# Kernel tuning notes

Measured on AMD Instinct MI355X. Metric: run time of the kernel, lower is better.

## Reference

```python
import jax, jax.numpy as jnp
import numpy as np

B, N, CIN, CV, D, H, HD, W, SHIFT = 1024, 192, 63, 27, 256, 8, 32, 8, 4
DEPTH, MLP = 2, 256  # mlp_dim = int(embed_dim * mlp_ratio) = 256


def setup_inputs() -> dict:
    key = jax.random.key(0)
    ks = iter(jax.random.split(key, 64))
    def w(*shape):
        return jax.random.normal(next(ks), shape, jnp.float32) * 0.02
    z = lambda *s: jnp.zeros(s, jnp.float32)
    o = lambda *s: jnp.ones(s, jnp.float32)
    return {
        'input_pts': jax.random.normal(next(ks), (B, N, CIN), jnp.float32),
        'input_views': jax.random.normal(next(ks), (B, CV), jnp.float32),
        'w_in': w(CIN, D), 'b_in': z(D),
        'ln_in_s': o(D), 'ln_in_b': z(D),
        'ln1_s': o(DEPTH, D), 'ln1_b': z(DEPTH, D),
        'wq': w(DEPTH, D, H, HD), 'bq': z(DEPTH, H, HD),
        'wk': w(DEPTH, D, H, HD), 'bk': z(DEPTH, H, HD),
        'wv': w(DEPTH, D, H, HD), 'bv': z(DEPTH, H, HD),
        'wo': w(DEPTH, H, HD, D), 'bo': z(DEPTH, D),
        'ln2_s': o(DEPTH, D), 'ln2_b': z(DEPTH, D),
        'w_mlp1': w(DEPTH, D, MLP), 'b_mlp1': z(DEPTH, MLP),
        'w_mlp2': w(DEPTH, MLP, D), 'b_mlp2': z(DEPTH, D),
        'w_skip': w(DEPTH, CIN + D, D), 'b_skip': z(DEPTH, D),
        'ln_f_s': o(D), 'ln_f_b': z(D),
        'w_alpha': w(D, 1), 'b_alpha': z(1),
        'w_feat': w(D, D), 'b_feat': z(D),
        'w_rgb1': w(D + CV, D // 2), 'b_rgb1': z(D // 2),
        'w_rgb2': w(D // 2, 3), 'b_rgb2': z(3),
    }


def _ln(x, s, b, eps=1e-6):
    m = jnp.mean(x, -1, keepdims=True)
    v = jnp.mean(jnp.square(x - m), -1, keepdims=True)
    return (x - m) * jax.lax.rsqrt(v + eps) * s + b


def _pos_embed(n, d):
    pos = jnp.arange(n, dtype=jnp.float32)[:, None]
    i = jnp.arange(d)
    ang = pos / jnp.power(10000.0, (2 * (i // 2)).astype(jnp.float32) / d)
    return jnp.where(i % 2 == 0, jnp.sin(ang), jnp.cos(ang))[None]  # [1, n, d]


def _block(x, shifted, ln1_s, ln1_b, wq, bq, wk, bk, wv, bv, wo, bo,
           ln2_s, ln2_b, w1, b1, w2, b2):
    b, n, c = x.shape
    y = _ln(x, ln1_s, ln1_b)
    if shifted:
        y = jnp.roll(y, -SHIFT, axis=1)
    yw = y.reshape(b * (n // W), W, c)  # window partition
    q = jnp.einsum('bnc,chd->bnhd', yw, wq) + bq
    k = jnp.einsum('bnc,chd->bnhd', yw, wk) + bk
    v = jnp.einsum('bnc,chd->bnhd', yw, wv) + bv
    scale = np.float32(1.0 / np.sqrt(HD))
    a = jax.nn.softmax(jnp.einsum('bqhd,bkhd->bhqk', q * scale, k), axis=-1)
    o = jnp.einsum('bhqk,bkhd->bqhd', a, v)
    o = jnp.einsum('bqhd,hdc->bqc', o, wo) + bo
    o = o.reshape(b, n, c)  # window reverse
    if shifted:
        o = jnp.roll(o, SHIFT, axis=1)
    x = x + o
    y = _ln(x, ln2_s, ln2_b)
    y = jax.nn.gelu(jnp.einsum('bnc,cm->bnm', y, w1) + b1)
    y = jnp.einsum('bnm,mc->bnc', y, w2) + b2
    return x + y


def reference(input_pts, input_views, w_in, b_in, ln_in_s, ln_in_b,
              ln1_s, ln1_b, wq, bq, wk, bk, wv, bv, wo, bo, ln2_s, ln2_b,
              w_mlp1, b_mlp1, w_mlp2, b_mlp2, w_skip, b_skip,
              ln_f_s, ln_f_b, w_alpha, b_alpha, w_feat, b_feat,
              w_rgb1, b_rgb1, w_rgb2, b_rgb2):
    x = input_pts @ w_in + b_in
    x = _ln(x, ln_in_s, ln_in_b)
    x = x + _pos_embed(x.shape[1], x.shape[2])
    for i in range(DEPTH):  # shift on odd layers; skips = [0, 1]
        x = _block(x, i % 2 == 1, ln1_s[i], ln1_b[i], wq[i], bq[i], wk[i], bk[i],
                   wv[i], bv[i], wo[i], bo[i], ln2_s[i], ln2_b[i],
                   w_mlp1[i], b_mlp1[i], w_mlp2[i], b_mlp2[i])
        x = jax.nn.gelu(jnp.concatenate([input_pts, x], -1) @ w_skip[i] + b_skip[i])
    h = _ln(x, ln_f_s, ln_f_b)
    alpha = h @ w_alpha + b_alpha
    feature = h @ w_feat + b_feat
    views = jnp.repeat(input_views[:, None, :], h.shape[1], axis=1)
    hr = jnp.concatenate([feature, views], -1)
    rgb = jax.nn.gelu(hr @ w_rgb1 + b_rgb1) @ w_rgb2 + b_rgb2
    return rgb, alpha
```

## Files before the change

kernel.cpp:

```cpp
#include <hip/hip_runtime.h>
#include <hip/hip_bf16.h>
#include <math.h>

typedef __hip_bfloat16 bf16;
typedef __attribute__((ext_vector_type(8))) short short8;
typedef __attribute__((ext_vector_type(4))) float f32x4;

#define T_TOK 196608
#define NSEQ  192
#define DMODEL 256
#define CHUNKS 4
#define CHUNKM (T_TOK/CHUNKS)

__device__ __forceinline__ float cvt(float v){ return v; }
__device__ __forceinline__ float cvt(bf16 v){ return __bfloat162float(v); }
__device__ __forceinline__ short bfbits(float f){
  bf16 h = __float2bfloat16(f); return *reinterpret_cast<short*>(&h);
}
__device__ __forceinline__ float blo(unsigned u){ return __uint_as_float(u << 16); }
__device__ __forceinline__ float bhi(unsigned u){ return __uint_as_float(u & 0xffff0000u); }
__device__ __forceinline__ float bfu(unsigned short v){ return __uint_as_float(((unsigned)v) << 16); }
__device__ __forceinline__ unsigned pack2(float a, float b){
  return ((unsigned)(unsigned short)bfbits(a)) | (((unsigned)(unsigned short)bfbits(b)) << 16);
}

__device__ __forceinline__ float gelu_f(float x){
  const float k0 = 0.7978845608028654f;
  return 0.5f*x*(1.0f + tanhf(k0*(x + 0.044715f*x*x*x)));
}

__global__ __launch_bounds__(256) void pe_kernel(float* __restrict__ PE){
  int n = blockIdx.x, d = threadIdx.x;
  float e = (float)(2*(d>>1)) / 256.f;
  float ang = (float)n * powf(10000.f, -e);
  PE[n*DMODEL + d] = (d & 1) ? cosf(ang) : sinf(ang);
}

__global__ __launch_bounds__(256) void w2b_kernel(
    const float* __restrict__ src, bf16* __restrict__ dst,
    int K, int N, int KL, int dstStride, int kOff)
{
  int idx = blockIdx.x*256 + threadIdx.x;
  if (idx >= N*KL) return;
  int n = idx / KL, k = idx - n*KL;
  dst[(size_t)n*dstStride + kOff + k] =
      __float2bfloat16(k < K ? src[(size_t)k*N + n] : 0.f);
}

__global__ __launch_bounds__(256) void pts2b_kernel(
    const float* __restrict__ src, bf16* __restrict__ dst)
{
  int idx = blockIdx.x*256 + threadIdx.x;
  int t = idx >> 6, k = idx & 63;
  dst[idx] = __float2bfloat16(k < 63 ? src[(size_t)t*63 + k] : 0.f);
}

__global__ __launch_bounds__(256) void views2b_kernel(
    const float* __restrict__ src, bf16* __restrict__ dst)
{
  int idx = blockIdx.x*256 + threadIdx.x;
  int t = idx >> 5, k = idx & 31;
  dst[idx] = __float2bfloat16(k < 27 ? src[(size_t)t*27 + k] : 0.f);
}

__global__ __launch_bounds__(256) void biascat_kernel(
    const float* __restrict__ b0, const float* __restrict__ b1,
    const float* __restrict__ b2, float* __restrict__ dst)
{
  int tid = threadIdx.x;
  const float* s = (blockIdx.x == 0) ? b0 : (blockIdx.x == 1) ? b1 : b2;
  dst[blockIdx.x*256 + tid] = s[tid];
}

__global__ __launch_bounds__(256) void ln_pe_kernel(
    bf16* __restrict__ X, const float* __restrict__ s, const float* __restrict__ b,
    const float* __restrict__ PE, float* __restrict__ s1o, float* __restrict__ s2o)
{
  const int lane = threadIdx.x & 63, w = threadIdx.x >> 6;
  const size_t t = (size_t)blockIdx.x * 4 + w;
  const int n = (int)(t % NSEQ);
  const int c = lane * 4;

  ushort4 u = *reinterpret_cast<const ushort4*>(X + t*DMODEL + c);
  float x0 = bfu(u.x), x1 = bfu(u.y), x2 = bfu(u.z), x3 = bfu(u.w);

  float sx = x0 + x1 + x2 + x3;
  float sq = x0*x0 + x1*x1 + x2*x2 + x3*x3;
  #pragma unroll
  for (int off = 32; off; off >>= 1){
    sx += __shfl_xor(sx, off, 64);
    sq += __shfl_xor(sq, off, 64);
  }
  float mean = sx * (1.f/256.f);
  float var  = sq * (1.f/256.f) - mean*mean;
  float rstd = rsqrtf(var + 1e-6f);

  float4 sv = *reinterpret_cast<const float4*>(s + c);
  float4 bv = *reinterpret_cast<const float4*>(b + c);
  float4 pv = *reinterpret_cast<const float4*>(PE + n*DMODEL + c);

  float y0 = (x0 - mean)*rstd*sv.x + bv.x + pv.x;
  float y1 = (x1 - mean)*rstd*sv.y + bv.y + pv.y;
  float y2 = (x2 - mean)*rstd*sv.z + bv.z + pv.z;
  float y3 = (x3 - mean)*rstd*sv.w + bv.w + pv.w;

  ushort4 o;
  o.x = (unsigned short)bfbits(y0);
  o.y = (unsigned short)bfbits(y1);
  o.z = (unsigned short)bfbits(y2);
  o.w = (unsigned short)bfbits(y3);
  *reinterpret_cast<ushort4*>(X + t*DMODEL + c) = o;

  float sy  = y0 + y1 + y2 + y3;
  float syq = y0*y0 + y1*y1 + y2*y2 + y3*y3;
  #pragma unroll
  for (int off = 32; off; off >>= 1){
    sy  += __shfl_xor(sy,  off, 64);
    syq += __shfl_xor(syq, off, 64);
  }
  if (lane == 0){ s1o[t] = sy; s2o[t] = syq; }
}

template<int MODE, bool ADD, bool GELU, bool STATS>
__global__ __launch_bounds__(256) void gemm_mfma(
    const bf16* __restrict__ A1, int lda1,
    const bf16* __restrict__ A2, int lda2, int SB, int aOff,
    const float* __restrict__ s1i, const float* __restrict__ s2i,
    const float* __restrict__ lnS, const float* __restrict__ lnB,
    const bf16* __restrict__ WT, int Kpad, const float* __restrict__ bias,
    bf16* __restrict__ C, int ldc, size_t segStride, int cOff, int rollShift,
    float* __restrict__ s1o, float* __restrict__ s2o)
{
  __shared__ short As[128*40];
  __shared__ short Cs[128*136];
  const int tid = threadIdx.x;
  const int lane = tid & 63, wid = tid >> 6;
  const int wm = wid >> 1, wn = wid & 1;
  const int col16 = lane & 15, quad = lane >> 4;
  const int m0 = blockIdx.y * 128, n0 = blockIdx.x * 128;
  const int sm = tid >> 1, half = tid & 1;

  f32x4 acc[4][4];
  #pragma unroll
  for (int i = 0; i < 4; i++)
    #pragma unroll
    for (int j = 0; j < 4; j++) acc[i][j] = (f32x4){0.f,0.f,0.f,0.f};

  int row = m0 + sm;
  if (MODE <= 1 && rollShift){
    int bb = row / NSEQ;
    int n  = row - bb*NSEQ;
    n += rollShift; if (n >= NSEQ) n -= NSEQ;
    row = bb*NSEQ + n;
  }
  const size_t arow = (size_t)aOff + row;
  const size_t arow2 = (MODE == 3) ? (arow / NSEQ) : arow;
  float lnMu = 0.f, lnRs = 0.f;
  if (MODE == 1){
    float m1 = s1i[arow] * (1.f/256.f);
    float m2 = s2i[arow] * (1.f/256.f);
    lnMu = m1;
    lnRs = rsqrtf(m2 - m1*m1 + 1e-6f);
  }

  for (int k0 = 0; k0 < Kpad; k0 += 32){
    const int gk = k0 + half*16;
    if (MODE == 1){
      const uint4 u0 = *(const uint4*)(A1 + arow*lda1 + gk);
      const uint4 u1 = *(const uint4*)(A1 + arow*lda1 + gk + 8);
      const unsigned uu[8] = {u0.x,u0.y,u0.z,u0.w,u1.x,u1.y,u1.z,u1.w};
      unsigned out[8];
      #pragma unroll
      for (int p = 0; p < 8; p++){
        int g = gk + 2*p;
        float a = (blo(uu[p]) - lnMu) * lnRs * lnS[g]   + lnB[g];
        float b = (bhi(uu[p]) - lnMu) * lnRs * lnS[g+1] + lnB[g+1];
        out[p] = pack2(a, b);
      }
      *(uint4*)&As[sm*40 + half*16]     = *(uint4*)&out[0];
      *(uint4*)&As[sm*40 + half*16 + 8] = *(uint4*)&out[4];
    } else {
      const bf16* src;
      if (MODE == 0) src = A1 + arow*lda1 + gk;
      else src = (gk < SB) ? (A1 + arow*(size_t)lda1 + gk)
                           : (A2 + arow2*(size_t)lda2 + (gk - SB));
      const uint4 u0 = *(const uint4*)(src);
      const uint4 u1 = *(const uint4*)(src + 8);
      *(uint4*)&As[sm*40 + half*16]     = u0;
      *(uint4*)&As[sm*40 + half*16 + 8] = u1;
    }
    __syncthreads();

    short8 afr[4];
    #pragma unroll
    for (int mi = 0; mi < 4; mi++)
      afr[mi] = *(const short8*)&As[(wm*64 + mi*16 + col16)*40 + quad*8];
    short8 bfr[4];
    #pragma unroll
    for (int ni = 0; ni < 4; ni++)
      bfr[ni] = *(const short8*)((const short*)WT
                 + (size_t)(n0 + wn*64 + ni*16 + col16)*Kpad + k0 + quad*8);
    #pragma unroll
    for (int mi = 0; mi < 4; mi++)
      #pragma unroll
      for (int ni = 0; ni < 4; ni++)
        acc[mi][ni] = __builtin_amdgcn_mfma_f32_16x16x32_bf16(
            afr[mi], bfr[ni], acc[mi][ni], 0, 0, 0);
    __syncthreads();
  }

  #pragma unroll
  for (int ni = 0; ni < 4; ni++){
    int ncol = wn*64 + ni*16 + col16;
    float bv = bias[n0 + ncol];
    #pragma unroll
    for (int mi = 0; mi < 4; mi++){
      f32x4 a = acc[mi][ni];
      #pragma unroll
      for (int r = 0; r < 4; r++){
        int lrow = wm*64 + mi*16 + quad*4 + r;
        float val = a[r] + bv;
        if (GELU) val = gelu_f(val);
        Cs[lrow*136 + ncol] = bfbits(val);
      }
    }
  }
  __syncthreads();

  const int seg = n0 >> 8;
  const int nb  = n0 & 255;
  const int orow = tid >> 4;
  const int ocol = (tid & 15) * 8;
  #pragma unroll
  for (int p = 0; p < 8; p++){
    int lrow = p*16 + orow;
    size_t mrow = (size_t)cOff + m0 + lrow;
    short8 v = *(const short8*)&Cs[lrow*136 + ocol];
    bf16* dst = C + (size_t)seg*segStride + mrow*ldc + nb + ocol;
    float rowSum = 0.f, rowSq = 0.f;
    if (ADD){
      short8 c = *(const short8*)dst;
      short8 o;
      #pragma unroll
      for (int e = 0; e < 8; e++){
        bf16 va, ca;
        *reinterpret_cast<short*>(&va) = v[e];
        *reinterpret_cast<short*>(&ca) = c[e];
        float f = cvt(va) + cvt(ca);
        o[e] = bfbits(f);
        if (STATS){ rowSum += f; rowSq += f*f; }
      }
      *(short8*)dst = o;
    } else {
      if (STATS){
        #pragma unroll
        for (int e = 0; e < 8; e++){
          bf16 va; *reinterpret_cast<short*>(&va) = v[e];
          float f = cvt(va);
          rowSum += f; rowSq += f*f;
        }
      }
      *(short8*)dst = v;
    }
    if (STATS){
      #pragma unroll
      for (int mk = 1; mk <= 8; mk <<= 1){
        rowSum += __shfl_xor(rowSum, mk, 64);
        rowSq  += __shfl_xor(rowSq,  mk, 64);
      }
      if ((tid & 15) == 0){
        atomicAdd(&s1o[mrow], rowSum);
        atomicAdd(&s2o[mrow], rowSq);
      }
    }
  }
}

__global__ __launch_bounds__(256) void attn_lite(
    bf16* __restrict__ Qg, const bf16* __restrict__ Kg, const bf16* __restrict__ Vg)
{
  __shared__ float qs[8][257], ks[8][257], vs[8][257];
  __shared__ float sc[8][8][8];
  const int c = threadIdx.x;
  const size_t base = (size_t)blockIdx.x * 8 * 256;
  #pragma unroll
  for (int j = 0; j < 8; j++){
    qs[j][c] = cvt(Qg[base + j*256 + c]);
    ks[j][c] = cvt(Kg[base + j*256 + c]);
    vs[j][c] = cvt(Vg[base + j*256 + c]);
  }
  __syncthreads();

  const float scale = 0.17677669529663687f;
  #pragma unroll
  for (int r = 0; r < 2; r++){
    int idx = r*256 + c;
    int h = idx >> 6, qi = (idx >> 3) & 7, ki = idx & 7;
    float s = 0.f;
    #pragma unroll
    for (int d = 0; d < 32; d++) s += qs[qi][h*32+d] * ks[ki][h*32+d];
    sc[h][qi][ki] = s * scale;
  }
  __syncthreads();

  if (c < 64){
    int h = c >> 3, qi = c & 7;
    float mx = -1e30f;
    #pragma unroll
    for (int u = 0; u < 8; u++) mx = fmaxf(mx, sc[h][qi][u]);
    float e[8], sum = 0.f;
    #pragma unroll
    for (int u = 0; u < 8; u++){ e[u] = __expf(sc[h][qi][u] - mx); sum += e[u]; }
    float inv = 1.f / sum;
    #pragma unroll
    for (int u = 0; u < 8; u++) sc[h][qi][u] = e[u] * inv;
  }
  __syncthreads();

  {
    int h = c >> 5;
    #pragma unroll
    for (int j = 0; j < 8; j++){
      float o = 0.f;
      #pragma unroll
      for (int u = 0; u < 8; u++) o += sc[h][j][u] * vs[u][c];
      Qg[base + j*256 + c] = __float2bfloat16(o);
    }
  }
}

__global__ __launch_bounds__(256) void alpha_kernel(
    const bf16* __restrict__ X, const float* __restrict__ s1,
    const float* __restrict__ s2, const float* __restrict__ s,
    const float* __restrict__ b, const float* __restrict__ wa,
    const float* __restrict__ ba, float* __restrict__ out)
{
  int lane = threadIdx.x & 63, w = threadIdx.x >> 6;
  size_t t = (size_t)blockIdx.x * 4 + w;
  float m = s1[t] * (1.f/256.f);
  float q = s2[t] * (1.f/256.f);
  float r = rsqrtf(q - m*m + 1e-6f);
  float acc = 0.f;
  #pragma unroll
  for (int j = 0; j < 4; j++){
    int c = lane + 64*j;
    float y = (cvt(X[t*DMODEL + c]) - m) * r * s[c] + b[c];
    acc += y * wa[c];
  }
  #pragma unroll
  for (int off = 32; off; off >>= 1) acc += __shfl_down(acc, off, 64);
  if (lane == 0) out[t] = acc + ba[0];
}

__global__ __launch_bounds__(256) void rgb2_kernel(
    const bf16* __restrict__ T1, const float* __restrict__ w2,
    const float* __restrict__ b2, float* __restrict__ out)
{
  int lane = threadIdx.x & 63, w = threadIdx.x >> 6;
  size_t t = (size_t)blockIdx.x * 4 + w;
  float h0 = cvt(T1[t*256 + lane]);
  float h1 = cvt(T1[t*256 + 64 + lane]);
  float a0 = h0*w2[lane*3+0] + h1*w2[(lane+64)*3+0];
  float a1 = h0*w2[lane*3+1] + h1*w2[(lane+64)*3+1];
  float a2 = h0*w2[lane*3+2] + h1*w2[(lane+64)*3+2];
  #pragma unroll
  for (int off = 32; off; off >>= 1){
    a0 += __shfl_down(a0, off, 64);
    a1 += __shfl_down(a1, off, 64);
    a2 += __shfl_down(a2, off, 64);
  }
  if (lane == 0){
    out[t*3+0] = a0 + b2[0];
    out[t*3+1] = a1 + b2[1];
    out[t*3+2] = a2 + b2[2];
  }
}

extern "C" void kernel_launch(void* const* d_in, const int* in_sizes, int n_in,
                              void* d_out, int out_size, void* d_ws, size_t ws_size,
                              hipStream_t stream)
{
  (void)in_sizes; (void)n_in; (void)out_size;
  const float* pts     = (const float*)d_in[0];
  const float* views   = (const float*)d_in[1];
  const float* w_in    = (const float*)d_in[2];
  const float* b_in    = (const float*)d_in[3];
  const float* ln_in_s = (const float*)d_in[4];
  const float* ln_in_b = (const float*)d_in[5];
  const float* ln1_s   = (const float*)d_in[6];
  const float* ln1_b   = (const float*)d_in[7];
  const float* wq      = (const float*)d_in[8];
  const float* bq      = (const float*)d_in[9];
  const float* wk      = (const float*)d_in[10];
  const float* bk      = (const float*)d_in[11];
  const float* wv      = (const float*)d_in[12];
  const float* bv      = (const float*)d_in[13];
  const float* wo      = (const float*)d_in[14];
  const float* bo      = (const float*)d_in[15];
  const float* ln2_s   = (const float*)d_in[16];
  const float* ln2_b   = (const float*)d_in[17];
  const float* w_mlp1  = (const float*)d_in[18];
  const float* b_mlp1  = (const float*)d_in[19];
  const float* w_mlp2  = (const float*)d_in[20];
  const float* b_mlp2  = (const float*)d_in[21];
  const float* w_skip  = (const float*)d_in[22];
  const float* b_skip  = (const float*)d_in[23];
  const float* ln_f_s  = (const float*)d_in[24];
  const float* ln_f_b  = (const float*)d_in[25];
  const float* w_alpha = (const float*)d_in[26];
  const float* b_alpha = (const float*)d_in[27];
  const float* w_feat  = (const float*)d_in[28];
  const float* b_feat  = (const float*)d_in[29];
  const float* w_rgb1  = (const float*)d_in[30];
  const float* b_rgb1  = (const float*)d_in[31];
  const float* w_rgb2  = (const float*)d_in[32];
  const float* b_rgb2  = (const float*)d_in[33];

  const size_t SZ = (size_t)T_TOK * DMODEL * 2;
  const size_t WT_ELEMS = 16384 + 2*(196608 + 3*65536 + 81920) + 65536 + 36864;
  const size_t NEED = 2*SZ + (size_t)4*T_TOK*4 + NSEQ*DMODEL*4 + 2*768*4
                    + WT_ELEMS*2 + (size_t)T_TOK*64*2 + 1024*32*2;
  if (ws_size < NEED) return;

  char* wsp = (char*)d_ws;
  bf16* xr = (bf16*)(wsp);
  bf16* x2 = (bf16*)(wsp + SZ);
  float* s1A = (float*)(wsp + 2*SZ);
  float* s2A = s1A + T_TOK;
  float* s1B = s2A + T_TOK;
  float* s2B = s1B + T_TOK;
  float* PE  = s2B + T_TOK;
  float* bqkv = PE + NSEQ*DMODEL;
  bf16* wtp = (bf16*)(bqkv + 2*768);

  bf16* wt_in = wtp;
  bf16* wt_qkv[2], *wt_o[2], *wt_m1[2], *wt_m2[2], *wt_sk[2];
  bf16* p = wt_in + 16384;
  for (int i = 0; i < 2; i++){
    wt_qkv[i] = p; p += 196608;
    wt_o[i]   = p; p += 65536;
    wt_m1[i]  = p; p += 65536;
    wt_m2[i]  = p; p += 65536;
    wt_sk[i]  = p; p += 81920;
  }
  bf16* wt_feat = p; p += 65536;
  bf16* wt_rgb1 = p; p += 36864;
  bf16* pts_b   = p; p += (size_t)T_TOK*64;
  bf16* views_b = p; p += 1024*32;

  float* out_rgb   = (float*)d_out;
  float* out_alpha = out_rgb + (size_t)T_TOK * 3;

  dim3 blk(256);
  dim3 g256(2, T_TOK/128);
  dim3 gQKV(6, CHUNKM/128);
  dim3 gC(2, CHUNKM/128);
  dim3 g128(1, T_TOK/128);
  dim3 gLN(T_TOK/4);
  dim3 gStat(T_TOK/4);
  dim3 gAttn(CHUNKM/8);

  const float* NF = nullptr;
  const bf16*  NB = nullptr;
  float* NFW = nullptr;

  pe_kernel<<<dim3(NSEQ), blk, 0, stream>>>(PE);
  pts2b_kernel<<<dim3(T_TOK*64/256), blk, 0, stream>>>(pts, pts_b);
  views2b_kernel<<<dim3(1024*32/256), blk, 0, stream>>>(views, views_b);
  #define W2B(src, dst, K_, N_, KL_, ST_, KO_) \
    w2b_kernel<<<dim3(((N_)*(KL_)+255)/256), blk, 0, stream>>>(src, dst, K_, N_, KL_, ST_, KO_)
  W2B(w_in, wt_in, 63, 256, 64, 64, 0);
  for (int i = 0; i < 2; i++){
    W2B(wq + (size_t)i*65536, wt_qkv[i],            256, 256, 256, 256, 0);
    W2B(wk + (size_t)i*65536, wt_qkv[i] + 65536,    256, 256, 256, 256, 0);
    W2B(wv + (size_t)i*65536, wt_qkv[i] + 131072,   256, 256, 256, 256, 0);
    W2B(wo + (size_t)i*65536, wt_o[i],  256, 256, 256, 256, 0);
    W2B(w_mlp1 + (size_t)i*65536, wt_m1[i], 256, 256, 256, 256, 0);
    W2B(w_mlp2 + (size_t)i*65536, wt_m2[i], 256, 256, 256, 256, 0);
    W2B(w_skip + (size_t)i*81664,            wt_sk[i], 63, 256, 64, 320, 0);
    W2B(w_skip + (size_t)i*81664 + 63*256,   wt_sk[i], 256, 256, 256, 320, 64);
    biascat_kernel<<<dim3(3), blk, 0, stream>>>(bq + i*256, bk + i*256, bv + i*256,
        bqkv + i*768);
  }
  W2B(w_feat, wt_feat, 256, 256, 256, 256, 0);
  W2B(w_rgb1,                wt_rgb1, 256, 128, 256, 288, 0);
  W2B(w_rgb1 + 256*128,      wt_rgb1, 27, 128, 32, 288, 256);
  #undef W2B

  gemm_mfma<0,false,false,false><<<g256, blk, 0, stream>>>(pts_b, 64, NB, 0, 0, 0,
      NF, NF, NF, NF, wt_in, 64, b_in, xr, 256, 0, 0, 0, NFW, NFW);
  ln_pe_kernel<<<gLN, blk, 0, stream>>>(xr, ln_in_s, ln_in_b, PE, s1A, s2A);

  for (int i = 0; i < 2; i++){
    const int shift = (i == 1) ? 4 : 0;
    const int shiftBack = (i == 1) ? (NSEQ - 4) : 0;

    hipMemsetAsync(s1B, 0, (size_t)2*T_TOK*4, stream);

    bf16* qb = x2;
    bf16* kb = x2 + (size_t)CHUNKM * 256;
    bf16* vb = x2 + (size_t)2 * CHUNKM * 256;
    for (int cch = 0; cch < CHUNKS; cch++){
      int base = cch * CHUNKM;
      gemm_mfma<1,false,false,false><<<gQKV, blk, 0, stream>>>(xr, 256, NB, 0, 0, base,
          s1A, s2A, ln1_s + i*256, ln1_b + i*256, wt_qkv[i], 256, bqkv + i*768,
          x2, 256, (size_t)CHUNKM*256, 0, shift, NFW, NFW);
      attn_lite<<<gAttn, blk, 0, stream>>>(qb, kb, vb);
      gemm_mfma<0,true,false,true><<<gC, blk, 0, stream>>>(qb, 256, NB, 0, 0, 0,
          NF, NF, NF, NF, wt_o[i], 256, bo + i*256, xr, 256, 0, base, shiftBack,
          s1B, s2B);
    }

    gemm_mfma<1,false,true ,false><<<g256, blk, 0, stream>>>(xr, 256, NB, 0, 0, 0,
        s1B, s2B, ln2_s + i*256, ln2_b + i*256, wt_m1[i], 256, b_mlp1 + i*256,
        x2, 256, 0, 0, 0, NFW, NFW);
    gemm_mfma<0,true ,false,false><<<g256, blk, 0, stream>>>(x2, 256, NB, 0, 0, 0,
        NF, NF, NF, NF, wt_m2[i], 256, b_mlp2 + i*256, xr, 256, 0, 0, 0, NFW, NFW);
    hipMemsetAsync(s1A, 0, (size_t)2*T_TOK*4, stream);
    gemm_mfma<2,false,true ,true><<<g256, blk, 0, stream>>>(pts_b, 64, xr, 256, 64, 0,
        NF, NF, NF, NF, wt_sk[i], 320, b_skip + i*256, x2, 256, 0, 0, 0,
        s1A, s2A);
    bf16* tmp = xr; xr = x2; x2 = tmp;
  }

  alpha_kernel<<<gStat, blk, 0, stream>>>(xr, s1A, s2A, ln_f_s, ln_f_b,
      w_alpha, b_alpha, out_alpha);
  gemm_mfma<1,false,false,false><<<g256, blk, 0, stream>>>(xr, 256, NB, 0, 0, 0,
      s1A, s2A, ln_f_s, ln_f_b, wt_feat, 256, b_feat, x2, 256, 0, 0, 0, NFW, NFW);
  gemm_mfma<3,false,true ,false><<<g128, blk, 0, stream>>>(x2, 256, views_b, 32, 256, 0,
      NF, NF, NF, NF, wt_rgb1, 288, b_rgb1, xr, 256, 0, 0, 0, NFW, NFW);
  rgb2_kernel<<<gStat, blk, 0, stream>>>(xr, w_rgb2, b_rgb2, out_rgb);
}
```

Baseline: 2.137 ms.

## Fold LayerNorm into GEMM weights and load A fragments directly from global

LayerNorm before the QKV, MLP1 and feature GEMMs is rewritten algebraically. The LN scale is folded into the bf16 weights, and per-column correction vectors u and wB are precomputed on the device. The mean/rstd correction is then applied in the epilogue, so the raw bf16 activations feed the MFMA directly. The GEMM also drops the LDS A tile and its two barriers per k-step, loading A and B fragments straight from global memory with a two-stage register double buffer. This removes per-element normalisation work and synchronisation, but the A rows are now read uncoalesced per lane and rounding behaviour shifts slightly.

```diff
diff --git a/kernel.cpp b/kernel.cpp
--- a/kernel.cpp
+++ b/kernel.cpp
@@ -17,12 +17,7 @@
 __device__ __forceinline__ short bfbits(float f){
   bf16 h = __float2bfloat16(f); return *reinterpret_cast<short*>(&h);
 }
-__device__ __forceinline__ float blo(unsigned u){ return __uint_as_float(u << 16); }
-__device__ __forceinline__ float bhi(unsigned u){ return __uint_as_float(u & 0xffff0000u); }
 __device__ __forceinline__ float bfu(unsigned short v){ return __uint_as_float(((unsigned)v) << 16); }
-__device__ __forceinline__ unsigned pack2(float a, float b){
-  return ((unsigned)(unsigned short)bfbits(a)) | (((unsigned)(unsigned short)bfbits(b)) << 16);
-}
 
 __device__ __forceinline__ float gelu_f(float x){
   const float k0 = 0.7978845608028654f;
@@ -38,13 +33,34 @@
 
 __global__ __launch_bounds__(256) void w2b_kernel(
     const float* __restrict__ src, bf16* __restrict__ dst,
-    int K, int N, int KL, int dstStride, int kOff)
+    int K, int N, int KL, int dstStride, int kOff, const float* __restrict__ scale)
 {
   int idx = blockIdx.x*256 + threadIdx.x;
   if (idx >= N*KL) return;
   int n = idx / KL, k = idx - n*KL;
-  dst[(size_t)n*dstStride + kOff + k] =
-      __float2bfloat16(k < K ? src[(size_t)k*N + n] : 0.f);
+  float v = 0.f;
+  if (k < K){
+    v = src[(size_t)k*N + n];
+    if (scale) v *= scale[k];
+  }
+  dst[(size_t)n*dstStride + kOff + k] = __float2bfloat16(v);
+}
+
+__global__ __launch_bounds__(256) void ucalc_kernel(
+    const float* __restrict__ W, const float* __restrict__ lnS,
+    const float* __restrict__ lnB, const float* __restrict__ bias,
+    float* __restrict__ u, float* __restrict__ wB, int K, int N)
+{
+  int n = blockIdx.x*256 + threadIdx.x;
+  if (n >= N) return;
+  float su = 0.f, sb = 0.f;
+  #pragma unroll 8
+  for (int k = 0; k < K; k++){
+    float w = W[(size_t)k*N + n];
+    su += cvt(__float2bfloat16(lnS[k]*w));
+    sb += lnB[k]*w;
+  }
+  u[n] = su; wB[n] = sb + bias[n];
 }
 
 __global__ __launch_bounds__(256) void pts2b_kernel(
@@ -61,15 +77,6 @@
   int idx = blockIdx.x*256 + threadIdx.x;
   int t = idx >> 5, k = idx & 31;
   dst[idx] = __float2bfloat16(k < 27 ? src[(size_t)t*27 + k] : 0.f);
-}
-
-__global__ __launch_bounds__(256) void biascat_kernel(
-    const float* __restrict__ b0, const float* __restrict__ b1,
-    const float* __restrict__ b2, float* __restrict__ dst)
-{
-  int tid = threadIdx.x;
-  const float* s = (blockIdx.x == 0) ? b0 : (blockIdx.x == 1) ? b1 : b2;
-  dst[blockIdx.x*256 + tid] = s[tid];
 }
 
 __global__ __launch_bounds__(256) void ln_pe_kernel(
@@ -121,24 +128,61 @@
   if (lane == 0){ s1o[t] = sy; s2o[t] = syq; }
 }
 
-template<int MODE, bool ADD, bool GELU, bool STATS>
+template<int MODE, bool LNF, bool ADD, bool GELU, bool STATS>
 __global__ __launch_bounds__(256) void gemm_mfma(
     const bf16* __restrict__ A1, int lda1,
     const bf16* __restrict__ A2, int lda2, int SB, int aOff,
     const float* __restrict__ s1i, const float* __restrict__ s2i,
-    const float* __restrict__ lnS, const float* __restrict__ lnB,
+    const float* __restrict__ uvec,
     const bf16* __restrict__ WT, int Kpad, const float* __restrict__ bias,
     bf16* __restrict__ C, int ldc, size_t segStride, int cOff, int rollShift,
     float* __restrict__ s1o, float* __restrict__ s2o)
 {
-  __shared__ short As[128*40];
   __shared__ short Cs[128*136];
+  __shared__ float sScale[128], sAlpha[128];
   const int tid = threadIdx.x;
   const int lane = tid & 63, wid = tid >> 6;
   const int wm = wid >> 1, wn = wid & 1;
   const int col16 = lane & 15, quad = lane >> 4;
   const int m0 = blockIdx.y * 128, n0 = blockIdx.x * 128;
-  const int sm = tid >> 1, half = tid & 1;
+
+  if (LNF){
+    if (tid < 128){
+      int row = m0 + tid;
+      if (rollShift){
+        int bb = row / NSEQ, n = row - bb*NSEQ;
+        n += rollShift; if (n >= NSEQ) n -= NSEQ;
+        row = bb*NSEQ + n;
+      }
+      size_t r = (size_t)aOff + row;
+      float m1 = s1i[r] * (1.f/256.f);
+      float m2 = s2i[r] * (1.f/256.f);
+      float rs = rsqrtf(m2 - m1*m1 + 1e-6f);
+      sScale[tid] = rs;
+      sAlpha[tid] = -m1*rs;
+    }
+  }
+
+  const bf16* ap1[4]; const bf16* ap2[4];
+  #pragma unroll
+  for (int mi = 0; mi < 4; mi++){
+    int row = m0 + wm*64 + mi*16 + col16;
+    if (MODE == 0 && rollShift){
+      int bb = row / NSEQ, n = row - bb*NSEQ;
+      n += rollShift; if (n >= NSEQ) n -= NSEQ;
+      row = bb*NSEQ + n;
+    }
+    size_t r1 = (size_t)aOff + row;
+    ap1[mi] = A1 + r1*(size_t)lda1 + quad*8;
+    if (MODE >= 2){
+      size_t r2 = (MODE == 3) ? (r1 / NSEQ) : r1;
+      ap2[mi] = A2 + r2*(size_t)lda2 + quad*8;
+    }
+  }
+  const bf16* bp[4];
+  #pragma unroll
+  for (int ni = 0; ni < 4; ni++)
+    bp[ni] = WT + (size_t)(n0 + wn*64 + ni*16 + col16)*Kpad + quad*8;
 
   f32x4 acc[4][4];
   #pragma unroll
@@ -146,80 +190,53 @@
     #pragma unroll
     for (int j = 0; j < 4; j++) acc[i][j] = (f32x4){0.f,0.f,0.f,0.f};
 
-  int row = m0 + sm;
-  if (MODE <= 1 && rollShift){
-    int bb = row / NSEQ;
-    int n  = row - bb*NSEQ;
-    n += rollShift; if (n >= NSEQ) n -= NSEQ;
-    row = bb*NSEQ + n;
-  }
-  const size_t arow = (size_t)aOff + row;
-  const size_t arow2 = (MODE == 3) ? (arow / NSEQ) : arow;
-  float lnMu = 0.f, lnRs = 0.f;
-  if (MODE == 1){
-    float m1 = s1i[arow] * (1.f/256.f);
-    float m2 = s2i[arow] * (1.f/256.f);
-    lnMu = m1;
-    lnRs = rsqrtf(m2 - m1*m1 + 1e-6f);
-  }
-
-  for (int k0 = 0; k0 < Kpad; k0 += 32){
-    const int gk = k0 + half*16;
-    if (MODE == 1){
-      const uint4 u0 = *(const uint4*)(A1 + arow*lda1 + gk);
-      const uint4 u1 = *(const uint4*)(A1 + arow*lda1 + gk + 8);
-      const unsigned uu[8] = {u0.x,u0.y,u0.z,u0.w,u1.x,u1.y,u1.z,u1.w};
-      unsigned out[8];
-      #pragma unroll
-      for (int p = 0; p < 8; p++){
-        int g = gk + 2*p;
-        float a = (blo(uu[p]) - lnMu) * lnRs * lnS[g]   + lnB[g];
-        float b = (bhi(uu[p]) - lnMu) * lnRs * lnS[g+1] + lnB[g+1];
-        out[p] = pack2(a, b);
-      }
-      *(uint4*)&As[sm*40 + half*16]     = *(uint4*)&out[0];
-      *(uint4*)&As[sm*40 + half*16 + 8] = *(uint4*)&out[4];
-    } else {
-      const bf16* src;
-      if (MODE == 0) src = A1 + arow*lda1 + gk;
-      else src = (gk < SB) ? (A1 + arow*(size_t)lda1 + gk)
-                           : (A2 + arow2*(size_t)lda2 + (gk - SB));
-      const uint4 u0 = *(const uint4*)(src);
-      const uint4 u1 = *(const uint4*)(src + 8);
-      *(uint4*)&As[sm*40 + half*16]     = u0;
-      *(uint4*)&As[sm*40 + half*16 + 8] = u1;
-    }
-    __syncthreads();
-
-    short8 afr[4];
-    #pragma unroll
-    for (int mi = 0; mi < 4; mi++)
-      afr[mi] = *(const short8*)&As[(wm*64 + mi*16 + col16)*40 + quad*8];
-    short8 bfr[4];
-    #pragma unroll
-    for (int ni = 0; ni < 4; ni++)
-      bfr[ni] = *(const short8*)((const short*)WT
-                 + (size_t)(n0 + wn*64 + ni*16 + col16)*Kpad + k0 + quad*8);
+  auto loadA = [&](int k0, short8* af){
+    #pragma unroll
+    for (int mi = 0; mi < 4; mi++){
+      const bf16* s;
+      if (MODE == 0) s = ap1[mi] + k0;
+      else s = (k0 < SB) ? (ap1[mi] + k0) : (ap2[mi] + (k0 - SB));
+      af[mi] = *(const short8*)s;
+    }
+  };
+  auto loadB = [&](int k0, short8* bf){
+    #pragma unroll
+    for (int ni = 0; ni < 4; ni++) bf[ni] = *(const short8*)(bp[ni] + k0);
+  };
+  auto domfma = [&](short8* af, short8* bf){
     #pragma unroll
     for (int mi = 0; mi < 4; mi++)
       #pragma unroll
       for (int ni = 0; ni < 4; ni++)
         acc[mi][ni] = __builtin_amdgcn_mfma_f32_16x16x32_bf16(
-            afr[mi], bfr[ni], acc[mi][ni], 0, 0, 0);
-    __syncthreads();
-  }
+            af[mi], bf[ni], acc[mi][ni], 0, 0, 0);
+  };
+
+  short8 aA[4], bA[4], aB[4], bB[4];
+  loadA(0, aA); loadB(0, bA);
+  for (int k0 = 0; k0 < Kpad; k0 += 64){
+    if (k0 + 32 < Kpad){ loadA(k0+32, aB); loadB(k0+32, bB); }
+    domfma(aA, bA);
+    if (k0 + 64 < Kpad){ loadA(k0+64, aA); loadB(k0+64, bA); }
+    if (k0 + 32 < Kpad) domfma(aB, bB);
+  }
+
+  if (LNF) __syncthreads();
 
   #pragma unroll
   for (int ni = 0; ni < 4; ni++){
     int ncol = wn*64 + ni*16 + col16;
     float bv = bias[n0 + ncol];
+    float uv = LNF ? uvec[n0 + ncol] : 0.f;
     #pragma unroll
     for (int mi = 0; mi < 4; mi++){
       f32x4 a = acc[mi][ni];
       #pragma unroll
       for (int r = 0; r < 4; r++){
         int lrow = wm*64 + mi*16 + quad*4 + r;
-        float val = a[r] + bv;
+        float val;
+        if (LNF) val = sScale[lrow]*a[r] + sAlpha[lrow]*uv + bv;
+        else     val = a[r] + bv;
         if (GELU) val = gelu_f(val);
         Cs[lrow*136 + ncol] = bfbits(val);
       }
@@ -418,7 +435,8 @@
 
   const size_t SZ = (size_t)T_TOK * DMODEL * 2;
   const size_t WT_ELEMS = 16384 + 2*(196608 + 3*65536 + 81920) + 65536 + 36864;
-  const size_t NEED = 2*SZ + (size_t)4*T_TOK*4 + NSEQ*DMODEL*4 + 2*768*4
+  const size_t UV_FLOATS = 2*768*2 + 2*256*2 + 2*256;
+  const size_t NEED = 2*SZ + (size_t)4*T_TOK*4 + NSEQ*DMODEL*4 + UV_FLOATS*4
                     + WT_ELEMS*2 + (size_t)T_TOK*64*2 + 1024*32*2;
   if (ws_size < NEED) return;
 
@@ -430,8 +448,18 @@
   float* s1B = s2A + T_TOK;
   float* s2B = s1B + T_TOK;
   float* PE  = s2B + T_TOK;
-  float* bqkv = PE + NSEQ*DMODEL;
-  bf16* wtp = (bf16*)(bqkv + 2*768);
+  float* uvp = PE + NSEQ*DMODEL;
+  float* uqkv[2], *wBqkv[2], *um1[2], *wBm1[2];
+  {
+    float* q = uvp;
+    for (int i = 0; i < 2; i++){ uqkv[i] = q; q += 768; }
+    for (int i = 0; i < 2; i++){ wBqkv[i] = q; q += 768; }
+    for (int i = 0; i < 2; i++){ um1[i] = q; q += 256; }
+    for (int i = 0; i < 2; i++){ wBm1[i] = q; q += 256; }
+  }
+  float* ufeat  = uvp + 2*768*2 + 2*256*2;
+  float* wBfeat = ufeat + 256;
+  bf16* wtp = (bf16*)(uvp + UV_FLOATS);
 
   bf16* wt_in = wtp;
   bf16* wt_qkv[2], *wt_o[2], *wt_m1[2], *wt_m2[2], *wt_sk[2];
@@ -461,34 +489,44 @@
   dim3 gAttn(CHUNKM/8);
 
   const float* NF = nullptr;
-  const bf16*  NB = nullptr;
   float* NFW = nullptr;
 
   pe_kernel<<<dim3(NSEQ), blk, 0, stream>>>(PE);
   pts2b_kernel<<<dim3(T_TOK*64/256), blk, 0, stream>>>(pts, pts_b);
   views2b_kernel<<<dim3(1024*32/256), blk, 0, stream>>>(views, views_b);
-  #define W2B(src, dst, K_, N_, KL_, ST_, KO_) \
-    w2b_kernel<<<dim3(((N_)*(KL_)+255)/256), blk, 0, stream>>>(src, dst, K_, N_, KL_, ST_, KO_)
-  W2B(w_in, wt_in, 63, 256, 64, 64, 0);
+  #define W2B(src, dst, K_, N_, KL_, ST_, KO_, SC_) \
+    w2b_kernel<<<dim3(((N_)*(KL_)+255)/256), blk, 0, stream>>>(src, dst, K_, N_, KL_, ST_, KO_, SC_)
+  W2B(w_in, wt_in, 63, 256, 64, 64, 0, NF);
   for (int i = 0; i < 2; i++){
-    W2B(wq + (size_t)i*65536, wt_qkv[i],            256, 256, 256, 256, 0);
-    W2B(wk + (size_t)i*65536, wt_qkv[i] + 65536,    256, 256, 256, 256, 0);
-    W2B(wv + (size_t)i*65536, wt_qkv[i] + 131072,   256, 256, 256, 256, 0);
-    W2B(wo + (size_t)i*65536, wt_o[i],  256, 256, 256, 256, 0);
-    W2B(w_mlp1 + (size_t)i*65536, wt_m1[i], 256, 256, 256, 256, 0);
-    W2B(w_mlp2 + (size_t)i*65536, wt_m2[i], 256, 256, 256, 256, 0);
-    W2B(w_skip + (size_t)i*81664,            wt_sk[i], 63, 256, 64, 320, 0);
-    W2B(w_skip + (size_t)i*81664 + 63*256,   wt_sk[i], 256, 256, 256, 320, 64);
-    biascat_kernel<<<dim3(3), blk, 0, stream>>>(bq + i*256, bk + i*256, bv + i*256,
-        bqkv + i*768);
-  }
-  W2B(w_feat, wt_feat, 256, 256, 256, 256, 0);
-  W2B(w_rgb1,                wt_rgb1, 256, 128, 256, 288, 0);
-  W2B(w_rgb1 + 256*128,      wt_rgb1, 27, 128, 32, 288, 256);
+    const float* s1 = ln1_s + i*256;
+    const float* b1 = ln1_b + i*256;
+    W2B(wq + (size_t)i*65536, wt_qkv[i],            256, 256, 256, 256, 0, s1);
+    W2B(wk + (size_t)i*65536, wt_qkv[i] + 65536,    256, 256, 256, 256, 0, s1);
+    W2B(wv + (size_t)i*65536, wt_qkv[i] + 131072,   256, 256, 256, 256, 0, s1);
+    ucalc_kernel<<<dim3(1), blk, 0, stream>>>(wq + (size_t)i*65536, s1, b1,
+        bq + i*256, uqkv[i],       wBqkv[i],       256, 256);
+    ucalc_kernel<<<dim3(1), blk, 0, stream>>>(wk + (size_t)i*65536, s1, b1,
+        bk + i*256, uqkv[i] + 256, wBqkv[i] + 256, 256, 256);
+    ucalc_kernel<<<dim3(1), blk, 0, stream>>>(wv + (size_t)i*65536, s1, b1,
+        bv + i*256, uqkv[i] + 512, wBqkv[i] + 512, 256, 256);
+    W2B(wo + (size_t)i*65536, wt_o[i],  256, 256, 256, 256, 0, NF);
+    W2B(w_mlp1 + (size_t)i*65536, wt_m1[i], 256, 256, 256, 256, 0, ln2_s + i*256);
+    ucalc_kernel<<<dim3(1), blk, 0, stream>>>(w_mlp1 + (size_t)i*65536,
+        ln2_s + i*256, ln2_b + i*256, b_mlp1 + i*256, um1[i], wBm1[i], 256, 256);
+    W2B(w_mlp2 + (size_t)i*65536, wt_m2[i], 256, 256, 256, 256, 0, NF);
+    W2B(w_skip + (size_t)i*81664,            wt_sk[i], 63, 256, 64, 320, 0, NF);
+    W2B(w_skip + (size_t)i*81664 + 63*256,   wt_sk[i], 256, 256, 256, 320, 64, NF);
+  }
+  W2B(w_feat, wt_feat, 256, 256, 256, 256, 0, ln_f_s);
+  ucalc_kernel<<<dim3(1), blk, 0, stream>>>(w_feat, ln_f_s, ln_f_b, b_feat,
+      ufeat, wBfeat, 256, 256);
+  W2B(w_rgb1,                wt_rgb1, 256, 128, 256, 288, 0, NF);
+  W2B(w_rgb1 + 256*128,      wt_rgb1, 27, 128, 32, 288, 256, NF);
   #undef W2B
 
-  gemm_mfma<0,false,false,false><<<g256, blk, 0, stream>>>(pts_b, 64, NB, 0, 0, 0,
-      NF, NF, NF, NF, wt_in, 64, b_in, xr, 256, 0, 0, 0, NFW, NFW);
+  gemm_mfma<0,false,false,false,false><<<g256, blk, 0, stream>>>(pts_b, 64,
+      (const bf16*)nullptr, 0, 0, 0, NF, NF, NF, wt_in, 64, b_in,
+      xr, 256, 0, 0, 0, NFW, NFW);
   ln_pe_kernel<<<gLN, blk, 0, stream>>>(xr, ln_in_s, ln_in_b, PE, s1A, s2A);
 
   for (int i = 0; i < 2; i++){
@@ -502,32 +540,37 @@
     bf16* vb = x2 + (size_t)2 * CHUNKM * 256;
     for (int cch = 0; cch < CHUNKS; cch++){
       int base = cch * CHUNKM;
-      gemm_mfma<1,false,false,false><<<gQKV, blk, 0, stream>>>(xr, 256, NB, 0, 0, base,
-          s1A, s2A, ln1_s + i*256, ln1_b + i*256, wt_qkv[i], 256, bqkv + i*768,
+      gemm_mfma<0,true,false,false,false><<<gQKV, blk, 0, stream>>>(xr, 256,
+          (const bf16*)nullptr, 0, 0, base, s1A, s2A, uqkv[i],
+          wt_qkv[i], 256, wBqkv[i],
           x2, 256, (size_t)CHUNKM*256, 0, shift, NFW, NFW);
       attn_lite<<<gAttn, blk, 0, stream>>>(qb, kb, vb);
-      gemm_mfma<0,true,false,true><<<gC, blk, 0, stream>>>(qb, 256, NB, 0, 0, 0,
-          NF, NF, NF, NF, wt_o[i], 256, bo + i*256, xr, 256, 0, base, shiftBack,
-          s1B, s2B);
-    }
-
-    gemm_mfma<1,false,true ,false><<<g256, blk, 0, stream>>>(xr, 256, NB, 0, 0, 0,
-        s1B, s2B, ln2_s + i*256, ln2_b + i*256, wt_m1[i], 256, b_mlp1 + i*256,
+      gemm_mfma<0,false,true,false,true><<<gC, blk, 0, stream>>>(qb, 256,
+          (const bf16*)nullptr, 0, 0, 0, NF, NF, NF, wt_o[i], 256, bo + i*256,
+          xr, 256, 0, base, shiftBack, s1B, s2B);
+    }
+
+    gemm_mfma<0,true,false,true,false><<<g256, blk, 0, stream>>>(xr, 256,
+        (const bf16*)nullptr, 0, 0, 0, s1B, s2B, um1[i],
+        wt_m1[i], 256, wBm1[i],
         x2, 256, 0, 0, 0, NFW, NFW);
-    gemm_mfma<0,true ,false,false><<<g256, blk, 0, stream>>>(x2, 256, NB, 0, 0, 0,
-        NF, NF, NF, NF, wt_m2[i], 256, b_mlp2 + i*256, xr, 256, 0, 0, 0, NFW, NFW);
+    gemm_mfma<0,false,true,false,false><<<g256, blk, 0, stream>>>(x2, 256,
+        (const bf16*)nullptr, 0, 0, 0, NF, NF, NF, wt_m2[i], 256, b_mlp2 + i*256,
+        xr, 256, 0, 0, 0, NFW, NFW);
     hipMemsetAsync(s1A, 0, (size_t)2*T_TOK*4, stream);
-    gemm_mfma<2,false,true ,true><<<g256, blk, 0, stream>>>(pts_b, 64, xr, 256, 64, 0,
-        NF, NF, NF, NF, wt_sk[i], 320, b_skip + i*256, x2, 256, 0, 0, 0,
-        s1A, s2A);
+    gemm_mfma<2,false,false,true,true><<<g256, blk, 0, stream>>>(pts_b, 64,
+        xr, 256, 64, 0, NF, NF, NF, wt_sk[i], 320, b_skip + i*256,
+        x2, 256, 0, 0, 0, s1A, s2A);
     bf16* tmp = xr; xr = x2; x2 = tmp;
   }
 
   alpha_kernel<<<gStat, blk, 0, stream>>>(xr, s1A, s2A, ln_f_s, ln_f_b,
       w_alpha, b_alpha, out_alpha);
-  gemm_mfma<1,false,false,false><<<g256, blk, 0, stream>>>(xr, 256, NB, 0, 0, 0,
-      s1A, s2A, ln_f_s, ln_f_b, wt_feat, 256, b_feat, x2, 256, 0, 0, 0, NFW, NFW);
-  gemm_mfma<3,false,true ,false><<<g128, blk, 0, stream>>>(x2, 256, views_b, 32, 256, 0,
-      NF, NF, NF, NF, wt_rgb1, 288, b_rgb1, xr, 256, 0, 0, 0, NFW, NFW);
+  gemm_mfma<0,true,false,false,false><<<g256, blk, 0, stream>>>(xr, 256,
+      (const bf16*)nullptr, 0, 0, 0, s1A, s2A, ufeat, wt_feat, 256, wBfeat,
+      x2, 256, 0, 0, 0, NFW, NFW);
+  gemm_mfma<3,false,false,true,false><<<g128, blk, 0, stream>>>(x2, 256,
+      views_b, 32, 256, 0, NF, NF, NF, wt_rgb1, 288, b_rgb1,
+      xr, 256, 0, 0, 0, NFW, NFW);
   rgb2_kernel<<<gStat, blk, 0, stream>>>(xr, w_rgb2, b_rgb2, out_rgb);
 }
```

Measured after the change: 2.442 ms. 14.3% more time.
